# Optimization experiments

Measured on AMD Instinct MI355X. Metric: run time of the kernel, lower is better.

The kernel has to match this reference:

```python
import jax, jax.numpy as jnp
import numpy as np

B, S, H, D = 2, 2048, 16, 64
E = H * D
ROPE_BASE = 10000.0


def rotate_half(x):
    x1 = x[..., ::2]
    x2 = x[..., 1::2]
    return jnp.concatenate((-x2, x1), axis=-1)


def rope_embeddings(seq_len, head_dim, base):
    inv_freq = 1.0 / base ** (jnp.arange(0, head_dim, 2, dtype=jnp.float32) / head_dim)
    pos = jnp.arange(seq_len, dtype=jnp.float32)
    freqs = jnp.outer(pos, inv_freq)  # (S, D/2)
    emb = jnp.concatenate((freqs, freqs), axis=-1)  # (S, D)
    return jnp.cos(emb)[None, :, None, :], jnp.sin(emb)[None, :, None, :]


def setup_inputs() -> dict:
    key = jax.random.key(0)
    ks = jax.random.split(key, 5)
    x = jax.random.normal(ks[0], (B, S, E), dtype=jnp.float32)
    # causal boolean mask: True = masked (disallowed)
    mask = ~jnp.tril(jnp.ones((S, S), dtype=bool))[None, None]
    scale = 1.0 / np.sqrt(E)
    Wq = jax.random.normal(ks[1], (E, E), dtype=jnp.float32) * scale
    Wk = jax.random.normal(ks[2], (E, E), dtype=jnp.float32) * scale
    Wv = jax.random.normal(ks[3], (E, E), dtype=jnp.float32) * scale
    Wo = jax.random.normal(ks[4], (E, E), dtype=jnp.float32) * scale
    return {"x": x, "mask": mask, "Wq": Wq, "Wk": Wk, "Wv": Wv, "Wo": Wo}


def reference(x, mask, Wq, Wk, Wv, Wo):
    b, s, e = x.shape
    q = (x @ Wq).reshape(b, s, H, D)
    k = (x @ Wk).reshape(b, s, H, D)
    v = (x @ Wv).reshape(b, s, H, D)
    cos_emb, sin_emb = rope_embeddings(s, D, ROPE_BASE)
    q = q * cos_emb + rotate_half(q) * sin_emb
    k = k * cos_emb + rotate_half(k) * sin_emb
    # (b, h, s_q, s_k)
    scores = jnp.einsum('bqhd,bkhd->bhqk', q, k) / jnp.sqrt(jnp.float32(D))
    mask_b = jnp.broadcast_to(mask, (b, H, s, s))
    scores = jnp.where(mask_b, jnp.finfo(jnp.float32).min, scores)
    attn = jax.nn.softmax(scores, axis=-1)
    out = jnp.einsum('bhqk,bkhd->bqhd', attn, v).reshape(b, s, e)
    return out @ Wo
```

## Files before the change

kernel.cpp:

```cpp
#include <hip/hip_runtime.h>

#define SEQ 2048
#define NH 16
#define HD 64
#define EMB 1024

typedef __attribute__((ext_vector_type(4))) float f32x4;
typedef __attribute__((ext_vector_type(16))) float f32x16;
typedef __attribute__((ext_vector_type(8))) __bf16 bf16x8;
typedef unsigned int u32x2 __attribute__((ext_vector_type(2)));
typedef unsigned int u32x4 __attribute__((ext_vector_type(4)));

__device__ inline unsigned short f2bf(float f){
  unsigned int u = __float_as_uint(f);
  return (unsigned short)((u + 0x7fffu + ((u >> 16) & 1u)) >> 16);
}
__device__ inline float bf2f(unsigned short h){ return __uint_as_float(((unsigned int)h) << 16); }

__device__ inline unsigned cvtpk(float lo, float hi){
  unsigned r;
  asm("v_cvt_pk_bf16_f32 %0, %1, %2" : "=v"(r) : "v"(lo), "v"(hi));
  return r;
}
__device__ inline u32x2 plswap(unsigned a, unsigned b){
  return __builtin_amdgcn_permlane32_swap(a, b, false, false);
}

__global__ __launch_bounds__(256) void k_convert(const float* __restrict__ in,
                                                 unsigned short* __restrict__ out, int n8){
  int i = blockIdx.x * 256 + threadIdx.x;
  if (i >= n8) return;
  const float4* p = (const float4*)in + (size_t)i * 2;
  float4 a = p[0], b = p[1];
  uint4 r;
  r.x = f2bf(a.x) | ((unsigned)f2bf(a.y) << 16);
  r.y = f2bf(a.z) | ((unsigned)f2bf(a.w) << 16);
  r.z = f2bf(b.x) | ((unsigned)f2bf(b.y) << 16);
  r.w = f2bf(b.z) | ((unsigned)f2bf(b.w) << 16);
  ((uint4*)out)[i] = r;
}

__global__ __launch_bounds__(256) void k_transpose_w(const float* __restrict__ Wq, const float* __restrict__ Wk,
                                                     const float* __restrict__ Wv, const float* __restrict__ Wo,
                                                     unsigned short* __restrict__ WtQKV,
                                                     unsigned short* __restrict__ WtO){
  int z = blockIdx.z;
  const float* W = (z == 0) ? Wq : (z == 1) ? Wk : (z == 2) ? Wv : Wo;
  unsigned short* out = (z < 3) ? (WtQKV + (size_t)z * EMB * EMB) : WtO;
  __shared__ float t[32][33];
  int n0 = blockIdx.x * 32, k0 = blockIdx.y * 32;
  int tx = threadIdx.x, ty = threadIdx.y;
  #pragma unroll
  for (int i = 0; i < 4; ++i)
    t[ty + i * 8][tx] = W[(size_t)(k0 + ty + i * 8) * EMB + n0 + tx];
  __syncthreads();
  #pragma unroll
  for (int i = 0; i < 4; ++i)
    out[(size_t)(n0 + ty + i * 8) * EMB + k0 + tx] = f2bf(t[tx][ty + i * 8]);
}

__global__ __launch_bounds__(256) void k_rope_table(float2* __restrict__ tb){
  int idx = blockIdx.x * 256 + threadIdx.x;
  int s = idx >> 5, j = idx & 31;
  float invf = __expf(-(float)j * (9.210340371976184f / 32.0f));
  float ang = (float)s * invf;
  tb[idx] = make_float2(cosf(ang), sinf(ang));
}

template<int MODE>
__global__ __launch_bounds__(256, 2) void k_gemm(const unsigned short* __restrict__ A,
                                                 const unsigned short* __restrict__ Bt,
                                                 unsigned short* __restrict__ Qb,
                                                 unsigned short* __restrict__ Kb,
                                                 unsigned short* __restrict__ Vb,
                                                 float* __restrict__ FO){
  const int Kd = 1024;
  int m0 = blockIdx.x * 128, n0 = blockIdx.y * 128;
  int tid = threadIdx.x;
  int w = tid >> 6, lane = tid & 63;
  int wm = w >> 1, wn = w & 1;
  int g = lane >> 4, lr = lane & 15;
  __shared__ unsigned short Ash[128 * 64];
  __shared__ unsigned short Bsh[128 * 64];
  f32x4 acc[4][4] = {};
  int r_ = tid >> 3, c_ = tid & 7;
  int rm = r_ & 7;
  int cc = c_ ^ rm;
  for (int kt = 0; kt < Kd / 64; ++kt){
    int kb = kt * 64;
    #pragma unroll
    for (int it = 0; it < 4; ++it){
      int row = it * 32 + r_;
      __builtin_amdgcn_global_load_lds(
        (const __attribute__((address_space(1))) void*)(A + (size_t)(m0 + row) * Kd + kb + cc * 8),
        (__attribute__((address_space(3))) void*)(Ash + it * 2048 + tid * 8), 16, 0, 0);
      __builtin_amdgcn_global_load_lds(
        (const __attribute__((address_space(1))) void*)(Bt + (size_t)(n0 + row) * Kd + kb + cc * 8),
        (__attribute__((address_space(3))) void*)(Bsh + it * 2048 + tid * 8), 16, 0, 0);
    }
    __syncthreads();
    #pragma unroll
    for (int kk = 0; kk < 2; ++kk){
      bf16x8 af[4], bfr[4];
      #pragma unroll
      for (int i = 0; i < 4; ++i){
        int ra = wm * 64 + i * 16 + lr;
        af[i]  = *(const bf16x8*)(Ash + ra * 64 + (((kk * 4 + g) ^ (ra & 7)) * 8));
        int rb = wn * 64 + i * 16 + lr;
        bfr[i] = *(const bf16x8*)(Bsh + rb * 64 + (((kk * 4 + g) ^ (rb & 7)) * 8));
      }
      #pragma unroll
      for (int mi = 0; mi < 4; ++mi)
        #pragma unroll
        for (int ni = 0; ni < 4; ++ni)
          acc[mi][ni] = __builtin_amdgcn_mfma_f32_16x16x32_bf16(af[mi], bfr[ni], acc[mi][ni], 0, 0, 0);
    }
    __syncthreads();
  }
  #pragma unroll
  for (int mi = 0; mi < 4; ++mi){
    #pragma unroll
    for (int ni = 0; ni < 4; ++ni){
      int col = n0 + wn * 64 + ni * 16 + lr;
      #pragma unroll
      for (int r = 0; r < 4; ++r){
        int mrow = m0 + wm * 64 + mi * 16 + 4 * g + r;
        float v = acc[mi][ni][r];
        if constexpr (MODE == 0){
          int mat = col >> 10, e = col & 1023;
          int h = e >> 6, d = e & 63;
          int bb = mrow >> 11, s = mrow & 2047;
          size_t off = ((size_t)((bb * NH + h) * SEQ + s)) * HD + d;
          if (mat == 0) v *= 0.18033688011112042f;
          unsigned short* dst = (mat == 0) ? Qb : (mat == 1) ? Kb : Vb;
          dst[off] = f2bf(v);
        } else {
          FO[(size_t)mrow * EMB + col] = v;
        }
      }
    }
  }
}

__global__ __launch_bounds__(64) void k_rope_frag(const unsigned short* __restrict__ Qin,
                                                  const unsigned short* __restrict__ Kin,
                                                  unsigned short* __restrict__ Qf,
                                                  unsigned short* __restrict__ Kf,
                                                  const float2* __restrict__ tb){
  int t = blockIdx.x, bh = blockIdx.y, z = blockIdx.z;
  const unsigned short* src = (z ? Kin : Qin) + ((size_t)bh * SEQ + t * 32) * HD;
  unsigned short* dst = z ? Kf : Qf;
  __shared__ __align__(16) unsigned char lds[32 * 160];
  int l = threadIdx.x, lr = l & 31, h = l >> 5;
  #pragma unroll
  for (int p = 0; p < 4; ++p){
    int i = p * 64 + l;
    uint4 g = ((const uint4*)src)[i];
    *(uint4*)(lds + (i >> 3) * 160 + (i & 7) * 16) = g;
  }
  __syncthreads();
  int srow = t * 32 + lr;
  #pragma unroll
  for (int d0 = 0; d0 < 4; ++d0){
    int j0 = (d0 & 1) * 16 + h * 8;
    bf16x8 own = *(const bf16x8*)(lds + lr * 160 + d0 * 32 + h * 16);
    bf16x8 plo = *(const bf16x8*)(lds + lr * 160 + (d0 & 1) * 64 + h * 32);
    bf16x8 phi = *(const bf16x8*)(lds + lr * 160 + (d0 & 1) * 64 + h * 32 + 16);
    bf16x8 part = (d0 < 2)
      ? __builtin_shufflevector(plo, phi, 1, 3, 5, 7, 9, 11, 13, 15)
      : __builtin_shufflevector(plo, phi, 0, 2, 4, 6, 8, 10, 12, 14);
    const float4* cp = (const float4*)(tb + (size_t)srow * 32 + j0);
    float4 c0 = cp[0], c1 = cp[1], c2 = cp[2], c3 = cp[3];
    float co[8] = {c0.x, c0.z, c1.x, c1.z, c2.x, c2.z, c3.x, c3.z};
    float si[8] = {c0.y, c0.w, c1.y, c1.w, c2.y, c2.w, c3.y, c3.w};
    float sg = (d0 < 2) ? -1.0f : 1.0f;
    unsigned w[4];
    #pragma unroll
    for (int i2 = 0; i2 < 4; ++i2){
      float e0 = (float)own[2 * i2]     * co[2 * i2]     + sg * (float)part[2 * i2]     * si[2 * i2];
      float e1 = (float)own[2 * i2 + 1] * co[2 * i2 + 1] + sg * (float)part[2 * i2 + 1] * si[2 * i2 + 1];
      w[i2] = (unsigned)f2bf(e0) | ((unsigned)f2bf(e1) << 16);
    }
    uint4 o; o.x = w[0]; o.y = w[1]; o.z = w[2]; o.w = w[3];
    ((uint4*)dst)[((size_t)(bh * 64 + t) * 4 + d0) * 64 + l] = o;
  }
}

__global__ __launch_bounds__(64) void k_vfrag(const unsigned short* __restrict__ V,
                                              unsigned short* __restrict__ Vf){
  int t = blockIdx.x, bh = blockIdx.y;
  const unsigned short* src = V + ((size_t)bh * SEQ + t * 32) * HD;
  __shared__ __align__(16) unsigned char lds[32 * 160];
  int l = threadIdx.x, lr = l & 31, h = l >> 5;
  #pragma unroll
  for (int p = 0; p < 4; ++p){
    int i = p * 64 + l;
    uint4 g = ((const uint4*)src)[i];
    *(uint4*)(lds + (i >> 3) * 160 + (i & 7) * 16) = g;
  }
  __syncthreads();
  #pragma unroll
  for (int dt = 0; dt < 2; ++dt){
    #pragma unroll
    for (int s2 = 0; s2 < 2; ++s2){
      unsigned w[4];
      #pragma unroll
      for (int i2 = 0; i2 < 4; ++i2){
        unsigned a = *(const unsigned short*)(lds + (s2 * 16 + h * 8 + 2 * i2) * 160 + (dt * 32 + lr) * 2);
        unsigned b = *(const unsigned short*)(lds + (s2 * 16 + h * 8 + 2 * i2 + 1) * 160 + (dt * 32 + lr) * 2);
        w[i2] = a | (b << 16);
      }
      uint4 o; o.x = w[0]; o.y = w[1]; o.z = w[2]; o.w = w[3];
      ((uint4*)Vf)[((size_t)(bh * 64 + t) * 4 + dt * 2 + s2) * 64 + l] = o;
    }
  }
}

#define MBIAS 8.0f

__global__ __launch_bounds__(128, 2) void k_attn(const unsigned short* __restrict__ Qf,
                                                 const unsigned short* __restrict__ Kf,
                                                 const unsigned short* __restrict__ Vf,
                                                 unsigned short* __restrict__ AO){
  int b0 = blockIdx.x;
  int bh = (b0 & 7) + 8 * (b0 >> 8);
  int p  = (b0 >> 3) & 31;
  int jA = p, jB = 63 - p;
  int q0A = jA * 32, q0B = jB * 32;
  int wid = threadIdx.x >> 6;
  int l = threadIdx.x & 63;
  int lr = l & 31, h = l >> 5;
  const unsigned short* Kp = Kf + (size_t)bh * 64 * 4 * 512;
  const unsigned short* Vp = Vf + (size_t)bh * 64 * 4 * 512;

  bf16x8 qfA[4], qfB[4];
  #pragma unroll
  for (int d0 = 0; d0 < 4; ++d0){
    qfA[d0] = *(const bf16x8*)(Qf + ((size_t)(bh * 64 + jA) * 4 + d0) * 512 + l * 8);
    qfB[d0] = *(const bf16x8*)(Qf + ((size_t)(bh * 64 + jB) * 4 + d0) * 512 + l * 8);
  }

  bf16x8 kf0[4], kf1[4], vf0[2][2], vf1[2][2];

  f32x16 oA0 = {}, oA1 = {}, oB0 = {}, oB1 = {};
  float lA = 0.f, lB = 0.f;

  auto LOADT = [&](bf16x8 (&kb)[4], bf16x8 (&vb)[2][2], int tt){
    const unsigned short* Kn = Kp + (size_t)tt * 4 * 512;
    const unsigned short* Vn = Vp + (size_t)tt * 4 * 512;
    #pragma unroll
    for (int d0 = 0; d0 < 4; ++d0)
      kb[d0] = *(const bf16x8*)(Kn + (size_t)d0 * 512 + l * 8);
    #pragma unroll
    for (int dt = 0; dt < 2; ++dt)
      #pragma unroll
      for (int s = 0; s < 2; ++s)
        vb[dt][s] = *(const bf16x8*)(Vn + (size_t)(dt * 2 + s) * 512 + l * 8);
  };

  auto PROC = [&](const bf16x8 (&kb)[4], const bf16x8 (&vb)[2][2], int tt){
    bool actA = (tt <= jA);
    __builtin_amdgcn_s_setprio(1);
    f32x16 stB, stA;
    #pragma unroll
    for (int r = 0; r < 16; ++r){ stB[r] = -MBIAS; stA[r] = -MBIAS; }
    #pragma unroll
    for (int d0 = 0; d0 < 4; ++d0)
      stB = __builtin_amdgcn_mfma_f32_32x32x16_bf16(kb[d0], qfB[d0], stB, 0, 0, 0);
    if (actA){
      #pragma unroll
      for (int d0 = 0; d0 < 4; ++d0)
        stA = __builtin_amdgcn_mfma_f32_32x32x16_bf16(kb[d0], qfA[d0], stA, 0, 0, 0);
    }
    __builtin_amdgcn_s_setprio(0);

    if (tt == jB){
      #pragma unroll
      for (int r = 0; r < 16; ++r){
        int kkl = (r & 3) + 8 * (r >> 2) + 4 * h;
        if (kkl > lr) stB[r] = -3.0e38f;
      }
    }
    #pragma unroll
    for (int r = 0; r < 16; ++r) stB[r] = exp2f(stB[r]);
    {
      float s8[8];
      #pragma unroll
      for (int r = 0; r < 8; ++r) s8[r] = stB[r] + stB[r + 8];
      #pragma unroll
      for (int r = 0; r < 4; ++r) s8[r] += s8[r + 4];
      lB += (s8[0] + s8[1]) + (s8[2] + s8[3]);
    }
    bf16x8 pfB[2];
    #pragma unroll
    for (int s = 0; s < 2; ++s){
      unsigned c0 = cvtpk(stB[8 * s + 0], stB[8 * s + 1]);
      unsigned c1 = cvtpk(stB[8 * s + 2], stB[8 * s + 3]);
      unsigned c2 = cvtpk(stB[8 * s + 4], stB[8 * s + 5]);
      unsigned c3 = cvtpk(stB[8 * s + 6], stB[8 * s + 7]);
      u32x2 r02 = plswap(c0, c2);
      u32x2 r13 = plswap(c1, c3);
      u32x4 uw;
      uw.x = r02.x; uw.y = r13.x; uw.z = r02.y; uw.w = r13.y;
      pfB[s] = __builtin_bit_cast(bf16x8, uw);
    }
    __builtin_amdgcn_s_setprio(1);
    #pragma unroll
    for (int s = 0; s < 2; ++s){
      oB0 = __builtin_amdgcn_mfma_f32_32x32x16_bf16(vb[0][s], pfB[s], oB0, 0, 0, 0);
      oB1 = __builtin_amdgcn_mfma_f32_32x32x16_bf16(vb[1][s], pfB[s], oB1, 0, 0, 0);
    }
    __builtin_amdgcn_s_setprio(0);

    if (actA){
      if (tt == jA){
        #pragma unroll
        for (int r = 0; r < 16; ++r){
          int kkl = (r & 3) + 8 * (r >> 2) + 4 * h;
          if (kkl > lr) stA[r] = -3.0e38f;
        }
      }
      #pragma unroll
      for (int r = 0; r < 16; ++r) stA[r] = exp2f(stA[r]);
      {
        float s8[8];
        #pragma unroll
        for (int r = 0; r < 8; ++r) s8[r] = stA[r] + stA[r + 8];
        #pragma unroll
        for (int r = 0; r < 4; ++r) s8[r] += s8[r + 4];
        lA += (s8[0] + s8[1]) + (s8[2] + s8[3]);
      }
      bf16x8 pfA[2];
      #pragma unroll
      for (int s = 0; s < 2; ++s){
        unsigned c0 = cvtpk(stA[8 * s + 0], stA[8 * s + 1]);
        unsigned c1 = cvtpk(stA[8 * s + 2], stA[8 * s + 3]);
        unsigned c2 = cvtpk(stA[8 * s + 4], stA[8 * s + 5]);
        unsigned c3 = cvtpk(stA[8 * s + 6], stA[8 * s + 7]);
        u32x2 r02 = plswap(c0, c2);
        u32x2 r13 = plswap(c1, c3);
        u32x4 uw;
        uw.x = r02.x; uw.y = r13.x; uw.z = r02.y; uw.w = r13.y;
        pfA[s] = __builtin_bit_cast(bf16x8, uw);
      }
      __builtin_amdgcn_s_setprio(1);
      #pragma unroll
      for (int s = 0; s < 2; ++s){
        oA0 = __builtin_amdgcn_mfma_f32_32x32x16_bf16(vb[0][s], pfA[s], oA0, 0, 0, 0);
        oA1 = __builtin_amdgcn_mfma_f32_32x32x16_bf16(vb[1][s], pfA[s], oA1, 0, 0, 0);
      }
      __builtin_amdgcn_s_setprio(0);
    }
  };

  LOADT(kf0, vf0, wid);
  for (int t = wid; t <= jB; t += 4){
    int t2 = (t + 2 > jB) ? jB : t + 2;
    LOADT(kf1, vf1, t2);
    PROC(kf0, vf0, t);
    int t4 = (t + 4 > jB) ? jB : t + 4;
    LOADT(kf0, vf0, t4);
    if (t + 2 <= jB) PROC(kf1, vf1, t + 2);
  }

  __shared__ float xch[66 * 64];
  if (wid == 1){
    #pragma unroll
    for (int r = 0; r < 16; ++r) xch[r * 64 + l]        = oA0[r];
    #pragma unroll
    for (int r = 0; r < 16; ++r) xch[(16 + r) * 64 + l] = oA1[r];
    #pragma unroll
    for (int r = 0; r < 16; ++r) xch[(32 + r) * 64 + l] = oB0[r];
    #pragma unroll
    for (int r = 0; r < 16; ++r) xch[(48 + r) * 64 + l] = oB1[r];
    xch[64 * 64 + l] = lA;
    xch[65 * 64 + l] = lB;
  }
  __syncthreads();
  if (wid == 0){
    #pragma unroll
    for (int r = 0; r < 16; ++r){
      oA0[r] += xch[r * 64 + l];
      oA1[r] += xch[(16 + r) * 64 + l];
      oB0[r] += xch[(32 + r) * 64 + l];
      oB1[r] += xch[(48 + r) * 64 + l];
    }
    lA += xch[64 * 64 + l];
    lB += xch[65 * 64 + l];

    int b = bh >> 4, hh = bh & 15;
    {
      u32x2 ss = plswap(__float_as_uint(lA), __float_as_uint(lA));
      float inv = 1.0f / (__uint_as_float(ss.x) + __uint_as_float(ss.y));
      unsigned short* outp = AO + ((size_t)(b * SEQ + q0A + lr)) * EMB + hh * HD;
      #pragma unroll
      for (int rq = 0; rq < 4; ++rq){
        uint2 wv;
        wv.x = cvtpk(oA0[rq * 4 + 0] * inv, oA0[rq * 4 + 1] * inv);
        wv.y = cvtpk(oA0[rq * 4 + 2] * inv, oA0[rq * 4 + 3] * inv);
        *(uint2*)(outp + 8 * rq + 4 * h) = wv;
      }
      #pragma unroll
      for (int rq = 0; rq < 4; ++rq){
        uint2 wv;
        wv.x = cvtpk(oA1[rq * 4 + 0] * inv, oA1[rq * 4 + 1] * inv);
        wv.y = cvtpk(oA1[rq * 4 + 2] * inv, oA1[rq * 4 + 3] * inv);
        *(uint2*)(outp + 32 + 8 * rq + 4 * h) = wv;
      }
    }
    {
      u32x2 ss = plswap(__float_as_uint(lB), __float_as_uint(lB));
      float inv = 1.0f / (__uint_as_float(ss.x) + __uint_as_float(ss.y));
      unsigned short* outp = AO + ((size_t)(b * SEQ + q0B + lr)) * EMB + hh * HD;
      #pragma unroll
      for (int rq = 0; rq < 4; ++rq){
        uint2 wv;
        wv.x = cvtpk(oB0[rq * 4 + 0] * inv, oB0[rq * 4 + 1] * inv);
        wv.y = cvtpk(oB0[rq * 4 + 2] * inv, oB0[rq * 4 + 3] * inv);
        *(uint2*)(outp + 8 * rq + 4 * h) = wv;
      }
      #pragma unroll
      for (int rq = 0; rq < 4; ++rq){
        uint2 wv;
        wv.x = cvtpk(oB1[rq * 4 + 0] * inv, oB1[rq * 4 + 1] * inv);
        wv.y = cvtpk(oB1[rq * 4 + 2] * inv, oB1[rq * 4 + 3] * inv);
        *(uint2*)(outp + 32 + 8 * rq + 4 * h) = wv;
      }
    }
  }
}

extern "C" void kernel_launch(void* const* d_in, const int* in_sizes, int n_in,
                              void* d_out, int out_size, void* d_ws, size_t ws_size,
                              hipStream_t stream){
  const float* x  = (const float*)d_in[0];
  const float* Wq = (const float*)d_in[2];
  const float* Wk = (const float*)d_in[3];
  const float* Wv = (const float*)d_in[4];
  const float* Wo = (const float*)d_in[5];
  float* out = (float*)d_out;

  char* ws = (char*)d_ws;
  size_t off = 0;
  auto alloc = [&](size_t bytes){ void* p = ws + off; off += (bytes + 255) & ~(size_t)255; return p; };
  unsigned short* xb    = (unsigned short*)alloc((size_t)4096 * 1024 * 2);
  unsigned short* wto   = (unsigned short*)alloc((size_t)1024 * 1024 * 2);
  unsigned short* qb    = (unsigned short*)alloc((size_t)4096 * 1024 * 2);
  unsigned short* kb    = (unsigned short*)alloc((size_t)4096 * 1024 * 2);
  unsigned short* vb    = (unsigned short*)alloc((size_t)4096 * 1024 * 2);
  float2*         tb    = (float2*)alloc((size_t)2048 * 32 * 8);
  unsigned short* wtqkv = (unsigned short*)alloc((size_t)4096 * 1024 * 2);
  unsigned short* Qf = xb;
  unsigned short* Kf = wtqkv;
  unsigned short* Vf = qb;
  unsigned short* ao = kb;

  k_convert<<<dim3(2048), dim3(256), 0, stream>>>(x, xb, 524288);
  k_transpose_w<<<dim3(32, 32, 4), dim3(32, 8), 0, stream>>>(Wq, Wk, Wv, Wo, wtqkv, wto);
  k_rope_table<<<dim3(256), dim3(256), 0, stream>>>(tb);
  k_gemm<0><<<dim3(32, 24), dim3(256), 0, stream>>>(xb, wtqkv, qb, kb, vb, nullptr);
  k_rope_frag<<<dim3(64, 32, 2), dim3(64), 0, stream>>>(qb, kb, Qf, Kf, tb);
  k_vfrag<<<dim3(64, 32), dim3(64), 0, stream>>>(vb, Vf);
  k_attn<<<dim3(1024), dim3(128), 0, stream>>>(Qf, Kf, Vf, ao);
  k_gemm<1><<<dim3(32, 8), dim3(256), 0, stream>>>(ao, wto, nullptr, nullptr, nullptr, out);
}
```

Before: 111.1 us.

## Fuse RoPE and fragment repacking into QKV GEMM epilogue

The QKV projection GEMM now stages its 128x128 output tile in shared memory per wave, then applies RoPE to Q/K and repacks Q, K and V directly into the attention fragment layouts. This removes the separate k_rope_frag and k_vfrag kernels and the intermediate bf16 Q/K/V round-trip through global memory, plus two launches. The trade-off is that shared memory per block grows to 42KB, which may limit occupancy of the GEMM, and the epilogue becomes heavier.

```diff
diff --git a/kernel.cpp b/kernel.cpp
--- a/kernel.cpp
+++ b/kernel.cpp
@@ -70,18 +70,20 @@
 template<int MODE>
 __global__ __launch_bounds__(256, 2) void k_gemm(const unsigned short* __restrict__ A,
                                                  const unsigned short* __restrict__ Bt,
-                                                 unsigned short* __restrict__ Qb,
-                                                 unsigned short* __restrict__ Kb,
-                                                 unsigned short* __restrict__ Vb,
-                                                 float* __restrict__ FO){
+                                                 unsigned short* __restrict__ Qf,
+                                                 unsigned short* __restrict__ Kf,
+                                                 unsigned short* __restrict__ Vf,
+                                                 float* __restrict__ FO,
+                                                 const float2* __restrict__ tb){
   const int Kd = 1024;
   int m0 = blockIdx.x * 128, n0 = blockIdx.y * 128;
   int tid = threadIdx.x;
   int w = tid >> 6, lane = tid & 63;
   int wm = w >> 1, wn = w & 1;
   int g = lane >> 4, lr = lane & 15;
-  __shared__ unsigned short Ash[128 * 64];
-  __shared__ unsigned short Bsh[128 * 64];
+  __shared__ __align__(16) unsigned char shm[43008];
+  unsigned short* Ash = (unsigned short*)shm;
+  unsigned short* Bsh = (unsigned short*)(shm + 16384);
   f32x4 acc[4][4] = {};
   int r_ = tid >> 3, c_ = tid & 7;
   int rm = r_ & 7;
@@ -117,101 +119,85 @@
     }
     __syncthreads();
   }
-  #pragma unroll
-  for (int mi = 0; mi < 4; ++mi){
-    #pragma unroll
-    for (int ni = 0; ni < 4; ++ni){
-      int col = n0 + wn * 64 + ni * 16 + lr;
-      #pragma unroll
-      for (int r = 0; r < 4; ++r){
-        int mrow = m0 + wm * 64 + mi * 16 + 4 * g + r;
-        float v = acc[mi][ni][r];
-        if constexpr (MODE == 0){
-          int mat = col >> 10, e = col & 1023;
-          int h = e >> 6, d = e & 63;
-          int bb = mrow >> 11, s = mrow & 2047;
-          size_t off = ((size_t)((bb * NH + h) * SEQ + s)) * HD + d;
-          if (mat == 0) v *= 0.18033688011112042f;
-          unsigned short* dst = (mat == 0) ? Qb : (mat == 1) ? Kb : Vb;
-          dst[off] = f2bf(v);
-        } else {
-          FO[(size_t)mrow * EMB + col] = v;
+
+  if constexpr (MODE == 1){
+    #pragma unroll
+    for (int mi = 0; mi < 4; ++mi){
+      #pragma unroll
+      for (int ni = 0; ni < 4; ++ni){
+        int col = n0 + wn * 64 + ni * 16 + lr;
+        #pragma unroll
+        for (int r = 0; r < 4; ++r){
+          int mrow = m0 + wm * 64 + mi * 16 + 4 * g + r;
+          FO[(size_t)mrow * EMB + col] = acc[mi][ni][r];
         }
       }
     }
-  }
-}
-
-__global__ __launch_bounds__(64) void k_rope_frag(const unsigned short* __restrict__ Qin,
-                                                  const unsigned short* __restrict__ Kin,
-                                                  unsigned short* __restrict__ Qf,
-                                                  unsigned short* __restrict__ Kf,
-                                                  const float2* __restrict__ tb){
-  int t = blockIdx.x, bh = blockIdx.y, z = blockIdx.z;
-  const unsigned short* src = (z ? Kin : Qin) + ((size_t)bh * SEQ + t * 32) * HD;
-  unsigned short* dst = z ? Kf : Qf;
-  __shared__ __align__(16) unsigned char lds[32 * 160];
-  int l = threadIdx.x, lr = l & 31, h = l >> 5;
-  #pragma unroll
-  for (int p = 0; p < 4; ++p){
-    int i = p * 64 + l;
-    uint4 g = ((const uint4*)src)[i];
-    *(uint4*)(lds + (i >> 3) * 160 + (i & 7) * 16) = g;
-  }
-  __syncthreads();
-  int srow = t * 32 + lr;
-  #pragma unroll
-  for (int d0 = 0; d0 < 4; ++d0){
-    int j0 = (d0 & 1) * 16 + h * 8;
-    bf16x8 own = *(const bf16x8*)(lds + lr * 160 + d0 * 32 + h * 16);
-    bf16x8 plo = *(const bf16x8*)(lds + lr * 160 + (d0 & 1) * 64 + h * 32);
-    bf16x8 phi = *(const bf16x8*)(lds + lr * 160 + (d0 & 1) * 64 + h * 32 + 16);
-    bf16x8 part = (d0 < 2)
-      ? __builtin_shufflevector(plo, phi, 1, 3, 5, 7, 9, 11, 13, 15)
-      : __builtin_shufflevector(plo, phi, 0, 2, 4, 6, 8, 10, 12, 14);
-    const float4* cp = (const float4*)(tb + (size_t)srow * 32 + j0);
-    float4 c0 = cp[0], c1 = cp[1], c2 = cp[2], c3 = cp[3];
-    float co[8] = {c0.x, c0.z, c1.x, c1.z, c2.x, c2.z, c3.x, c3.z};
-    float si[8] = {c0.y, c0.w, c1.y, c1.w, c2.y, c2.w, c3.y, c3.w};
-    float sg = (d0 < 2) ? -1.0f : 1.0f;
-    unsigned w[4];
-    #pragma unroll
-    for (int i2 = 0; i2 < 4; ++i2){
-      float e0 = (float)own[2 * i2]     * co[2 * i2]     + sg * (float)part[2 * i2]     * si[2 * i2];
-      float e1 = (float)own[2 * i2 + 1] * co[2 * i2 + 1] + sg * (float)part[2 * i2 + 1] * si[2 * i2 + 1];
-      w[i2] = (unsigned)f2bf(e0) | ((unsigned)f2bf(e1) << 16);
-    }
-    uint4 o; o.x = w[0]; o.y = w[1]; o.z = w[2]; o.w = w[3];
-    ((uint4*)dst)[((size_t)(bh * 64 + t) * 4 + d0) * 64 + l] = o;
-  }
-}
-
-__global__ __launch_bounds__(64) void k_vfrag(const unsigned short* __restrict__ V,
-                                              unsigned short* __restrict__ Vf){
-  int t = blockIdx.x, bh = blockIdx.y;
-  const unsigned short* src = V + ((size_t)bh * SEQ + t * 32) * HD;
-  __shared__ __align__(16) unsigned char lds[32 * 160];
-  int l = threadIdx.x, lr = l & 31, h = l >> 5;
-  #pragma unroll
-  for (int p = 0; p < 4; ++p){
-    int i = p * 64 + l;
-    uint4 g = ((const uint4*)src)[i];
-    *(uint4*)(lds + (i >> 3) * 160 + (i & 7) * 16) = g;
-  }
-  __syncthreads();
-  #pragma unroll
-  for (int dt = 0; dt < 2; ++dt){
-    #pragma unroll
-    for (int s2 = 0; s2 < 2; ++s2){
-      unsigned w[4];
-      #pragma unroll
-      for (int i2 = 0; i2 < 4; ++i2){
-        unsigned a = *(const unsigned short*)(lds + (s2 * 16 + h * 8 + 2 * i2) * 160 + (dt * 32 + lr) * 2);
-        unsigned b = *(const unsigned short*)(lds + (s2 * 16 + h * 8 + 2 * i2 + 1) * 160 + (dt * 32 + lr) * 2);
-        w[i2] = a | (b << 16);
-      }
-      uint4 o; o.x = w[0]; o.y = w[1]; o.z = w[2]; o.w = w[3];
-      ((uint4*)Vf)[((size_t)(bh * 64 + t) * 4 + dt * 2 + s2) * 64 + l] = o;
+  } else {
+    unsigned char* tile = shm + w * 10752;
+    int mat = n0 >> 10;
+    float scl = (mat == 0) ? 0.18033688011112042f : 1.0f;
+    #pragma unroll
+    for (int mi = 0; mi < 4; ++mi)
+      #pragma unroll
+      for (int ni = 0; ni < 4; ++ni)
+        #pragma unroll
+        for (int r = 0; r < 4; ++r)
+          *(unsigned short*)(tile + (mi * 16 + 4 * g + r) * 168 + (ni * 16 + lr) * 2)
+              = f2bf(acc[mi][ni][r] * scl);
+    __syncthreads();
+    int l32 = lane & 31, h2 = lane >> 5;
+    int rowbase = m0 + wm * 64;
+    int bb = rowbase >> 11, sbase = rowbase & 2047;
+    int hd = ((n0 & 1023) >> 6) + wn;
+    size_t tbase = (size_t)((bb * NH + hd) * 64 + (sbase >> 5));
+    if (mat < 2){
+      unsigned short* dst = mat ? Kf : Qf;
+      #pragma unroll
+      for (int tt = 0; tt < 2; ++tt){
+        int srow = sbase + tt * 32 + l32;
+        const unsigned char* base = tile + (tt * 32 + l32) * 168;
+        #pragma unroll
+        for (int d0 = 0; d0 < 4; ++d0){
+          bf16x8 own = *(const bf16x8*)(base + d0 * 32 + h2 * 16);
+          bf16x8 plo = *(const bf16x8*)(base + (d0 & 1) * 64 + h2 * 32);
+          bf16x8 phi = *(const bf16x8*)(base + (d0 & 1) * 64 + h2 * 32 + 16);
+          bf16x8 part = (d0 < 2)
+            ? __builtin_shufflevector(plo, phi, 1, 3, 5, 7, 9, 11, 13, 15)
+            : __builtin_shufflevector(plo, phi, 0, 2, 4, 6, 8, 10, 12, 14);
+          const float4* cp = (const float4*)(tb + (size_t)srow * 32 + (d0 & 1) * 16 + h2 * 8);
+          float4 c0 = cp[0], c1 = cp[1], c2 = cp[2], c3 = cp[3];
+          float co[8] = {c0.x, c0.z, c1.x, c1.z, c2.x, c2.z, c3.x, c3.z};
+          float si[8] = {c0.y, c0.w, c1.y, c1.w, c2.y, c2.w, c3.y, c3.w};
+          float sg = (d0 < 2) ? -1.0f : 1.0f;
+          unsigned wv[4];
+          #pragma unroll
+          for (int i2 = 0; i2 < 4; ++i2){
+            float e0 = (float)own[2 * i2]     * co[2 * i2]     + sg * (float)part[2 * i2]     * si[2 * i2];
+            float e1 = (float)own[2 * i2 + 1] * co[2 * i2 + 1] + sg * (float)part[2 * i2 + 1] * si[2 * i2 + 1];
+            wv[i2] = (unsigned)f2bf(e0) | ((unsigned)f2bf(e1) << 16);
+          }
+          uint4 o; o.x = wv[0]; o.y = wv[1]; o.z = wv[2]; o.w = wv[3];
+          ((uint4*)dst)[((tbase + tt) * 4 + d0) * 64 + lane] = o;
+        }
+      }
+    } else {
+      #pragma unroll
+      for (int tt = 0; tt < 2; ++tt)
+        #pragma unroll
+        for (int dt = 0; dt < 2; ++dt)
+          #pragma unroll
+          for (int s2 = 0; s2 < 2; ++s2){
+            unsigned wv[4];
+            #pragma unroll
+            for (int i2 = 0; i2 < 4; ++i2){
+              unsigned a = *(const unsigned short*)(tile + (tt * 32 + s2 * 16 + h2 * 8 + 2 * i2) * 168 + (dt * 32 + l32) * 2);
+              unsigned b = *(const unsigned short*)(tile + (tt * 32 + s2 * 16 + h2 * 8 + 2 * i2 + 1) * 168 + (dt * 32 + l32) * 2);
+              wv[i2] = a | (b << 16);
+            }
+            uint4 o; o.x = wv[0]; o.y = wv[1]; o.z = wv[2]; o.w = wv[3];
+            ((uint4*)Vf)[((tbase + tt) * 4 + dt * 2 + s2) * 64 + lane] = o;
+          }
     }
   }
 }
@@ -444,23 +430,18 @@
   size_t off = 0;
   auto alloc = [&](size_t bytes){ void* p = ws + off; off += (bytes + 255) & ~(size_t)255; return p; };
   unsigned short* xb    = (unsigned short*)alloc((size_t)4096 * 1024 * 2);
+  unsigned short* wtqkv = (unsigned short*)alloc((size_t)3072 * 1024 * 2);
   unsigned short* wto   = (unsigned short*)alloc((size_t)1024 * 1024 * 2);
-  unsigned short* qb    = (unsigned short*)alloc((size_t)4096 * 1024 * 2);
-  unsigned short* kb    = (unsigned short*)alloc((size_t)4096 * 1024 * 2);
-  unsigned short* vb    = (unsigned short*)alloc((size_t)4096 * 1024 * 2);
   float2*         tb    = (float2*)alloc((size_t)2048 * 32 * 8);
-  unsigned short* wtqkv = (unsigned short*)alloc((size_t)4096 * 1024 * 2);
-  unsigned short* Qf = xb;
-  unsigned short* Kf = wtqkv;
-  unsigned short* Vf = qb;
-  unsigned short* ao = kb;
+  unsigned short* Qf    = (unsigned short*)alloc((size_t)4096 * 1024 * 2);
+  unsigned short* Kf    = (unsigned short*)alloc((size_t)4096 * 1024 * 2);
+  unsigned short* Vf    = (unsigned short*)alloc((size_t)4096 * 1024 * 2);
+  unsigned short* ao = xb;
 
   k_convert<<<dim3(2048), dim3(256), 0, stream>>>(x, xb, 524288);
   k_transpose_w<<<dim3(32, 32, 4), dim3(32, 8), 0, stream>>>(Wq, Wk, Wv, Wo, wtqkv, wto);
   k_rope_table<<<dim3(256), dim3(256), 0, stream>>>(tb);
-  k_gemm<0><<<dim3(32, 24), dim3(256), 0, stream>>>(xb, wtqkv, qb, kb, vb, nullptr);
-  k_rope_frag<<<dim3(64, 32, 2), dim3(64), 0, stream>>>(qb, kb, Qf, Kf, tb);
-  k_vfrag<<<dim3(64, 32), dim3(64), 0, stream>>>(vb, Vf);
+  k_gemm<0><<<dim3(32, 24), dim3(256), 0, stream>>>(xb, wtqkv, Qf, Kf, Vf, nullptr, tb);
   k_attn<<<dim3(1024), dim3(128), 0, stream>>>(Qf, Kf, Vf, ao);
-  k_gemm<1><<<dim3(32, 8), dim3(256), 0, stream>>>(ao, wto, nullptr, nullptr, nullptr, out);
-}
+  k_gemm<1><<<dim3(32, 8), dim3(256), 0, stream>>>(ao, wto, nullptr, nullptr, nullptr, out, nullptr);
+}
```

After: 100.7 us. 9.4% less time.
